# Kernel optimization log

Measured on AMD Instinct MI355X. Metric: run time of the kernel, lower is better.

## Reference

```python
import jax, jax.numpy as jnp
import numpy as np

B, T, D = 64, 256, 1024
H, HS = 16, 64
FF = 4096
EPS = 1e-5


def _layernorm(x, g, b):
    mu = jnp.mean(x, axis=-1, keepdims=True)
    var = jnp.mean(jnp.square(x - mu), axis=-1, keepdims=True)
    return (x - mu) * jax.lax.rsqrt(var + EPS) * g + b


def setup_inputs() -> dict:
    key = jax.random.key(0)
    ks = jax.random.split(key, 12)
    s = 0.02
    return {
        "x": jax.random.normal(ks[0], (B, T, D), jnp.float32),
        "ln1_g": jnp.ones((D,), jnp.float32),
        "ln1_b": jnp.zeros((D,), jnp.float32),
        "Wq": jax.random.normal(ks[1], (H, D, HS), jnp.float32) * s,
        "Wk": jax.random.normal(ks[2], (H, D, HS), jnp.float32) * s,
        "Wv": jax.random.normal(ks[3], (H, D, HS), jnp.float32) * s,
        "Wproj": jax.random.normal(ks[4], (D, D), jnp.float32) * s,
        "bproj": jnp.zeros((D,), jnp.float32),
        "ln2_g": jnp.ones((D,), jnp.float32),
        "ln2_b": jnp.zeros((D,), jnp.float32),
        "W1": jax.random.normal(ks[5], (D, FF), jnp.float32) * s,
        "b1": jnp.zeros((FF,), jnp.float32),
        "W2": jax.random.normal(ks[6], (FF, D), jnp.float32) * s,
        "b2": jnp.zeros((D,), jnp.float32),
    }


def reference(x, ln1_g, ln1_b, Wq, Wk, Wv, Wproj, bproj, ln2_g, ln2_b, W1, b1, W2, b2):
    # x = ln1(x)
    h = _layernorm(x, ln1_g, ln1_b)
    # per-head Q/K/V projections, batched over heads
    q = jnp.einsum("btd,hde->bhte", h, Wq)
    k = jnp.einsum("btd,hde->bhte", h, Wk)
    v = jnp.einsum("btd,hde->bhte", h, Wv)
    # NOTE: source scales by C**-0.5 with C = input_size (D), not head_size
    scale = D ** -0.5
    scores = jnp.einsum("bhte,bhse->bhts", q, k) * scale
    causal = jnp.tril(jnp.ones((T, T), bool))
    scores = jnp.where(causal, scores, -jnp.inf)
    w = jax.nn.softmax(scores, axis=-1)  # dropout is identity in eval
    attn = jnp.einsum("bhts,bhse->bthe", w, v).reshape(x.shape[0], x.shape[1], H * HS)
    sa = attn @ Wproj + bproj
    # residual onto ln1 output (as written in source)
    y = h + sa
    h2 = _layernorm(y, ln2_g, ln2_b)
    ff = jax.nn.relu(h2 @ W1 + b1) @ W2 + b2
    return h2 + ff
```

## Files before the change

kernel.cpp:

```cpp
#include <hip/hip_runtime.h>

typedef __bf16 bf16x8 __attribute__((ext_vector_type(8)));
typedef float f32x4 __attribute__((ext_vector_type(4)));
typedef unsigned short ushort_t;

__device__ __forceinline__ ushort_t f2bf(float f) {
  unsigned int u = __float_as_uint(f);
  u += 0x7fffu + ((u >> 16) & 1u);
  return (ushort_t)(u >> 16);
}

__device__ __forceinline__ void gl_lds16(const ushort_t* g, const char* l) {
  __builtin_amdgcn_global_load_lds(
      (const __attribute__((address_space(1))) void*)g,
      (__attribute__((address_space(3))) void*)l, 16, 0, 0);
}

__global__ __launch_bounds__(256) void fill_k(float* __restrict__ p, long n, float v) {
  long i = (long)blockIdx.x * 256 + threadIdx.x;
  if (i < n) p[i] = v;
}

__global__ __launch_bounds__(256) void transpose_w(const float* __restrict__ in,
                                                   ushort_t* __restrict__ out,
                                                   int R, int C) {
  __shared__ float tile[32][33];
  const float* inb = in + (long)blockIdx.z * R * C;
  ushort_t* outb = out + (long)blockIdx.z * R * C;
  int r0 = blockIdx.x * 32, c0 = blockIdx.y * 32;
  int tx = threadIdx.x & 31, ty = threadIdx.x >> 5;
#pragma unroll
  for (int i = ty; i < 32; i += 8) tile[i][tx] = inb[(long)(r0 + i) * C + (c0 + tx)];
  __syncthreads();
#pragma unroll
  for (int i = ty; i < 32; i += 8) outb[(long)(c0 + i) * R + (r0 + tx)] = f2bf(tile[tx][i]);
}

__global__ __launch_bounds__(256) void ln_k(const float* __restrict__ x,
                                            const float* __restrict__ g,
                                            const float* __restrict__ b,
                                            float* __restrict__ outF,
                                            ushort_t* __restrict__ outU) {
  __shared__ float red[8];
  long row = blockIdx.x;
  int tid = threadIdx.x;
  float4 v = ((const float4*)(x + row * 1024))[tid];
  float s = v.x + v.y + v.z + v.w;
#pragma unroll
  for (int off = 32; off; off >>= 1) s += __shfl_xor(s, off);
  int w = tid >> 6;
  if ((tid & 63) == 0) red[w] = s;
  __syncthreads();
  float mean = (red[0] + red[1] + red[2] + red[3]) * (1.0f / 1024.0f);
  float dx = v.x - mean, dy = v.y - mean, dz = v.z - mean, dw = v.w - mean;
  float s2 = dx * dx + dy * dy + dz * dz + dw * dw;
#pragma unroll
  for (int off = 32; off; off >>= 1) s2 += __shfl_xor(s2, off);
  if ((tid & 63) == 0) red[4 + w] = s2;
  __syncthreads();
  float var = (red[4] + red[5] + red[6] + red[7]) * (1.0f / 1024.0f);
  float rstd = rsqrtf(var + 1e-5f);
  int c = tid * 4;
  float o0 = dx * rstd * g[c + 0] + b[c + 0];
  float o1 = dy * rstd * g[c + 1] + b[c + 1];
  float o2 = dz * rstd * g[c + 2] + b[c + 2];
  float o3 = dw * rstd * g[c + 3] + b[c + 3];
  ((float4*)(outF + row * 1024))[tid] = make_float4(o0, o1, o2, o3);
  ushort4 u;
  u.x = f2bf(o0); u.y = f2bf(o1); u.z = f2bf(o2); u.w = f2bf(o3);
  ((ushort4*)(outU + row * 1024))[tid] = u;
}

template <int EPI>
__global__ __launch_bounds__(512, 2) void gemm256(const ushort_t* __restrict__ A,
                                                  const ushort_t* __restrict__ Bt,
                                                  int M, int N, int K, int NBC,
                                                  const float* __restrict__ bias,
                                                  const float* res, float* outF,
                                                  ushort_t* __restrict__ outU,
                                                  ushort_t* __restrict__ outU2,
                                                  ushort_t* __restrict__ outU3) {
  __shared__ __align__(16) char lds[131072];
  const int tid = threadIdx.x;
  const int lane = tid & 63;
  const int w = tid >> 6;
  const int wr = w >> 2, wc = w & 3;
  const int g = lane >> 4, lr = lane & 15;
  const int cpx = gridDim.x >> 3;
  const int wg = (blockIdx.x & 7) * cpx + (blockIdx.x >> 3);
  const long m0 = (long)(wg / NBC) * 256;
  const long n0 = (long)(wg % NBC) * 256;
  const int srow = tid >> 3;
  const int sslot = (tid & 7) ^ (srow & 7);
  const ushort_t* sA = A + (m0 + srow) * (long)K + sslot * 8;
  const ushort_t* sB = Bt + (n0 + srow) * (long)K + sslot * 8;
  const int dA = tid * 16;
  const int dB = 32768 + tid * 16;
  const int abase = (wr * 128 + lr) * 128;
  const int bbase = 32768 + (wc * 64 + lr) * 128;
  const int s0 = g ^ (lr & 7);
  const int s1 = (4 + g) ^ (lr & 7);
  const int NT = K >> 6;

  f32x4 acc[8][4] = {};
  bf16x8 aR[4][2], bR[4][2];
  const char* rb;

#define STAGE_A(tile, half) do {                                          \
    const long _ko = (long)(tile) * 64;                                   \
    char* _d = lds + (((tile) & 1) << 16) + ((half) << 14) + dA;          \
    gl_lds16(sA + _ko + (long)(2 * (half)) * 64 * K, _d);                 \
    gl_lds16(sA + _ko + (long)(2 * (half) + 1) * 64 * K, _d + 8192);      \
  } while (0)
#define STAGE_B(tile, half) do {                                          \
    const long _ko = (long)(tile) * 64;                                   \
    char* _d = lds + (((tile) & 1) << 16) + ((half) << 14) + dB;          \
    gl_lds16(sB + _ko + (long)(2 * (half)) * 64 * K, _d);                 \
    gl_lds16(sB + _ko + (long)(2 * (half) + 1) * 64 * K, _d + 8192);      \
  } while (0)
#define RD_A(base_mf) do {                                                \
    _Pragma("unroll") for (int mf = 0; mf < 4; ++mf) {                    \
      aR[mf][0] = *(const bf16x8*)(rb + abase + ((base_mf) + mf) * 2048 + s0 * 16); \
      aR[mf][1] = *(const bf16x8*)(rb + abase + ((base_mf) + mf) * 2048 + s1 * 16); \
    } } while (0)
#define RD_B2(base_nf) do {                                               \
    _Pragma("unroll") for (int nf = 0; nf < 2; ++nf) {                    \
      bR[(base_nf) + nf][0] = *(const bf16x8*)(rb + bbase + ((base_nf) + nf) * 2048 + s0 * 16); \
      bR[(base_nf) + nf][1] = *(const bf16x8*)(rb + bbase + ((base_nf) + nf) * 2048 + s1 * 16); \
    } } while (0)
#define QUAD(MB, NB) do {                                                 \
    __builtin_amdgcn_s_setprio(1);                                        \
    _Pragma("unroll") for (int mf = 0; mf < 4; ++mf)                      \
      _Pragma("unroll") for (int nf = 0; nf < 2; ++nf) {                  \
        acc[(MB) + mf][(NB) + nf] = __builtin_amdgcn_mfma_f32_16x16x32_bf16(aR[mf][0], bR[(NB) + nf][0], acc[(MB) + mf][(NB) + nf], 0, 0, 0); \
        acc[(MB) + mf][(NB) + nf] = __builtin_amdgcn_mfma_f32_16x16x32_bf16(aR[mf][1], bR[(NB) + nf][1], acc[(MB) + mf][(NB) + nf], 0, 0, 0); \
      }                                                                   \
    __builtin_amdgcn_s_setprio(0); } while (0)
#define LGKM0 do {                                                        \
    asm volatile("s_waitcnt lgkmcnt(0)" ::: "memory");                    \
    __builtin_amdgcn_sched_barrier(0); } while (0)

  STAGE_B(0, 0); STAGE_B(0, 1); STAGE_A(0, 0); STAGE_A(0, 1);
  STAGE_B(1, 0); STAGE_B(1, 1); STAGE_A(1, 0);
  asm volatile("s_waitcnt vmcnt(6)" ::: "memory");
  __builtin_amdgcn_s_barrier();

  for (int t = 0; t < NT; t += 2) {
    const bool s2 = (t + 2 < NT), s3 = (t + 3 < NT);
    rb = lds;
    RD_A(0);
    RD_B2(0);
    STAGE_A(t + 1, 1);
    asm volatile("s_waitcnt lgkmcnt(8)" ::: "memory");
    __builtin_amdgcn_s_barrier();
    LGKM0;
    QUAD(0, 0);
    __builtin_amdgcn_s_barrier();
    RD_B2(2);
    __builtin_amdgcn_s_barrier();
    LGKM0;
    QUAD(0, 2);
    __builtin_amdgcn_s_barrier();
    if (s2) STAGE_B(t + 2, 0);
    RD_A(4);
    __builtin_amdgcn_s_barrier();
    LGKM0;
    QUAD(4, 2);
    __builtin_amdgcn_s_barrier();
    if (s2) { STAGE_B(t + 2, 1); STAGE_A(t + 2, 0); }
    __builtin_amdgcn_s_barrier();
    QUAD(4, 0);
    if (s2) asm volatile("s_waitcnt vmcnt(6)" ::: "memory");
    else    asm volatile("s_waitcnt vmcnt(0)" ::: "memory");
    __builtin_amdgcn_s_barrier();
    rb = lds + 65536;
    RD_A(0);
    RD_B2(0);
    if (s2) STAGE_A(t + 2, 1);
    asm volatile("s_waitcnt lgkmcnt(8)" ::: "memory");
    __builtin_amdgcn_s_barrier();
    LGKM0;
    QUAD(0, 0);
    __builtin_amdgcn_s_barrier();
    RD_B2(2);
    __builtin_amdgcn_s_barrier();
    LGKM0;
    QUAD(0, 2);
    __builtin_amdgcn_s_barrier();
    if (s3) STAGE_B(t + 3, 0);
    RD_A(4);
    __builtin_amdgcn_s_barrier();
    LGKM0;
    QUAD(4, 2);
    __builtin_amdgcn_s_barrier();
    if (s3) { STAGE_B(t + 3, 1); STAGE_A(t + 3, 0); }
    __builtin_amdgcn_s_barrier();
    QUAD(4, 0);
    if (s3) asm volatile("s_waitcnt vmcnt(6)" ::: "memory");
    else    asm volatile("s_waitcnt vmcnt(0)" ::: "memory");
    __builtin_amdgcn_s_barrier();
  }
#undef STAGE_A
#undef STAGE_B
#undef RD_A
#undef RD_B2
#undef QUAD
#undef LGKM0

  if constexpr (EPI == 4) {
    const int p = (int)(n0 >> 10);
    const long bb2 = m0 >> 8;
    if (p < 2) {
      ushort_t* dst = (p == 0) ? outU : outU2;
#pragma unroll
      for (int mf = 0; mf < 8; ++mf)
#pragma unroll
        for (int nf = 0; nf < 4; ++nf)
#pragma unroll
          for (int r = 0; r < 4; ++r) {
            long tt = (wr * 128 + mf * 16 + g * 4 + r);
            long cc = (n0 & 1023) + wc * 64 + nf * 16 + lr;
            long hh = cc >> 6, e = cc & 63;
            dst[(((bb2 * 16 + hh) * 256 + tt) << 6) + e] = f2bf(acc[mf][nf][r]);
          }
    } else {
      unsigned int* l32 = (unsigned int*)lds;
#pragma unroll
      for (int mf = 0; mf < 8; ++mf)
#pragma unroll
        for (int nf = 0; nf < 4; ++nf)
#pragma unroll
          for (int r2 = 0; r2 < 2; ++r2) {
            int row = wr * 128 + mf * 16 + g * 4 + r2 * 2;
            int col = wc * 64 + nf * 16 + lr;
            unsigned int pk = (unsigned int)f2bf(acc[mf][nf][r2 * 2]) |
                              ((unsigned int)f2bf(acc[mf][nf][r2 * 2 + 1]) << 16);
            l32[col * 128 + ((row >> 1) ^ ((col & 7) << 2))] = pk;
          }
      __syncthreads();
      const long vcol0 = (n0 & 1023);
#pragma unroll
      for (int k = 0; k < 16; ++k) {
        int c = tid + k * 512;
        int e_l = c >> 5, k16 = c & 31;
        uint4 d = *(uint4*)&l32[e_l * 128 + ((k16 * 4) ^ ((e_l & 7) << 2))];
        long vc = vcol0 + e_l;
        long hh = vc >> 6, e = vc & 63;
        *(uint4*)&outU3[(((bb2 * 16 + hh) * 64 + e) << 8) + k16 * 8] = d;
      }
    }
  } else {
#pragma unroll
    for (int mf = 0; mf < 8; ++mf)
#pragma unroll
      for (int nf = 0; nf < 4; ++nf)
#pragma unroll
        for (int r = 0; r < 4; ++r) {
          long row = m0 + wr * 128 + mf * 16 + g * 4 + r;
          long col = n0 + wc * 64 + nf * 16 + lr;
          float v = acc[mf][nf][r];
          if constexpr (EPI == 2) {
            long i = row * N + col;
            outF[i] = v + bias[col] + res[i];
          } else {
            outU[row * N + col] = f2bf(fmaxf(v + bias[col], 0.0f));
          }
        }
  }
}

__global__ __launch_bounds__(64, 4) void attn_k(const ushort_t* __restrict__ q,
                                                const ushort_t* __restrict__ k,
                                                const ushort_t* __restrict__ vt,
                                                ushort_t* __restrict__ ao) {
  __shared__ __align__(16) ushort_t Ps[32][40];
  const int lane = threadIdx.x;
  const int g = lane >> 4, lr = lane & 15;
  const int blk = blockIdx.x;
  const int q8 = blk & 7;
  const int bh = blk >> 3;
  const int bb = bh >> 4, hh = bh & 15;
  const int q0 = q8 * 32;
  const ushort_t* qb = q + (long)bh * 256 * 64;
  const ushort_t* kb = k + (long)bh * 256 * 64;
  const ushort_t* vb = vt + (long)bh * 64 * 256;
  bf16x8 qf[2][2];
#pragma unroll
  for (int m = 0; m < 2; m++)
#pragma unroll
    for (int ks = 0; ks < 2; ks++)
      qf[m][ks] = *(const bf16x8*)(qb + (q0 + m * 16 + lr) * 64 + ks * 32 + g * 8);
  f32x4 o[2][4] = {};
  float mrow[2][4], lrow[2][4];
#pragma unroll
  for (int m = 0; m < 2; m++)
#pragma unroll
    for (int r = 0; r < 4; r++) { mrow[m][r] = -3.0e38f; lrow[m][r] = 0.0f; }
  const float sc2 = 0.04508422f;
  const int nkb = q8 + 1;
  for (int kbk = 0; kbk < nkb; kbk++) {
    f32x4 s[2][2] = {};
#pragma unroll
    for (int ks = 0; ks < 2; ks++) {
      bf16x8 kf[2];
#pragma unroll
      for (int n = 0; n < 2; n++)
        kf[n] = *(const bf16x8*)(kb + (kbk * 32 + n * 16 + lr) * 64 + ks * 32 + g * 8);
#pragma unroll
      for (int m = 0; m < 2; m++)
#pragma unroll
        for (int n = 0; n < 2; n++)
          s[m][n] = __builtin_amdgcn_mfma_f32_16x16x32_bf16(qf[m][ks], kf[n], s[m][n], 0, 0, 0);
    }
    bf16x8 vf[4];
#pragma unroll
    for (int n = 0; n < 4; n++)
      vf[n] = *(const bf16x8*)(vb + (n * 16 + lr) * 256 + kbk * 32 + g * 8);
    if (kbk == q8) {
#pragma unroll
      for (int m = 0; m < 2; m++)
#pragma unroll
        for (int n = 0; n < 2; n++)
#pragma unroll
          for (int r = 0; r < 4; r++) {
            int row = q0 + m * 16 + g * 4 + r;
            int col = kbk * 32 + n * 16 + lr;
            s[m][n][r] = (col <= row) ? s[m][n][r] * sc2 : -3.0e38f;
          }
    } else {
#pragma unroll
      for (int m = 0; m < 2; m++)
#pragma unroll
        for (int n = 0; n < 2; n++)
#pragma unroll
          for (int r = 0; r < 4; r++) s[m][n][r] *= sc2;
    }
    float mx[2][4];
    float growth = -3.0e38f;
#pragma unroll
    for (int m = 0; m < 2; m++)
#pragma unroll
      for (int r = 0; r < 4; r++) {
        float v = fmaxf(s[m][0][r], s[m][1][r]);
#pragma unroll
        for (int off = 8; off; off >>= 1) v = fmaxf(v, __shfl_xor(v, off));
        mx[m][r] = v;
        growth = fmaxf(growth, v - mrow[m][r]);
      }
    if (__any(growth > 8.0f)) {
#pragma unroll
      for (int m = 0; m < 2; m++)
#pragma unroll
        for (int r = 0; r < 4; r++) {
          float mn = fmaxf(mrow[m][r], mx[m][r]);
          float al = exp2f(mrow[m][r] - mn);
          mrow[m][r] = mn;
          lrow[m][r] *= al;
#pragma unroll
          for (int n = 0; n < 4; n++) o[m][n][r] *= al;
        }
    }
#pragma unroll
    for (int m = 0; m < 2; m++)
#pragma unroll
      for (int r = 0; r < 4; r++) {
        float rs = 0.0f;
#pragma unroll
        for (int n = 0; n < 2; n++) {
          float p = exp2f(s[m][n][r] - mrow[m][r]);
          s[m][n][r] = p;
          rs += p;
        }
#pragma unroll
        for (int off = 8; off; off >>= 1) rs += __shfl_xor(rs, off);
        lrow[m][r] += rs;
      }
#pragma unroll
    for (int m = 0; m < 2; m++)
#pragma unroll
      for (int n = 0; n < 2; n++)
#pragma unroll
        for (int r = 0; r < 4; r++)
          Ps[m * 16 + g * 4 + r][n * 16 + lr] = f2bf(s[m][n][r]);
#pragma unroll
    for (int m = 0; m < 2; m++) {
      bf16x8 pa = *(const bf16x8*)&Ps[m * 16 + lr][g * 8];
#pragma unroll
      for (int n = 0; n < 4; n++)
        o[m][n] = __builtin_amdgcn_mfma_f32_16x16x32_bf16(pa, vf[n], o[m][n], 0, 0, 0);
    }
  }
#pragma unroll
  for (int m = 0; m < 2; m++)
#pragma unroll
    for (int r = 0; r < 4; r++) {
      float inv = 1.0f / lrow[m][r];
      long t = q0 + m * 16 + g * 4 + r;
#pragma unroll
      for (int n = 0; n < 4; n++) {
        long e = n * 16 + lr;
        ao[((long)bb * 256 + t) * 1024 + hh * 64 + e] = f2bf(o[m][n][r] * inv);
      }
    }
}

extern "C" void kernel_launch(void* const* d_in, const int* in_sizes, int n_in,
                              void* d_out, int out_size, void* d_ws, size_t ws_size,
                              hipStream_t stream) {
  const float* x     = (const float*)d_in[0];
  const float* ln1g  = (const float*)d_in[1];
  const float* ln1b  = (const float*)d_in[2];
  const float* Wq    = (const float*)d_in[3];
  const float* Wk    = (const float*)d_in[4];
  const float* Wv    = (const float*)d_in[5];
  const float* Wproj = (const float*)d_in[6];
  const float* bproj = (const float*)d_in[7];
  const float* ln2g  = (const float*)d_in[8];
  const float* ln2b  = (const float*)d_in[9];
  const float* W1    = (const float*)d_in[10];
  const float* b1    = (const float*)d_in[11];
  const float* W2    = (const float*)d_in[12];
  const float* b2    = (const float*)d_in[13];

  const long NEED = 184L << 20;
  if (ws_size < (size_t)NEED) {
    fill_k<<<(out_size + 255) / 256, 256, 0, stream>>>((float*)d_out, out_size,
                                                       (float)(ws_size >> 20));
    return;
  }

  char* ws = (char*)d_ws;
  const long MB = 1 << 20;
  ushort_t* wqt = (ushort_t*)(ws + 0 * MB);
  ushort_t* wkt = (ushort_t*)(ws + 2 * MB);
  ushort_t* wvt = (ushort_t*)(ws + 4 * MB);
  ushort_t* wpt = (ushort_t*)(ws + 6 * MB);
  ushort_t* w1t = (ushort_t*)(ws + 8 * MB);
  ushort_t* w2t = (ushort_t*)(ws + 16 * MB);
  ushort_t* hb  = (ushort_t*)(ws + 24 * MB);
  ushort_t* qbf = (ushort_t*)(ws + 56 * MB);
  ushort_t* kbf = (ushort_t*)(ws + 88 * MB);
  ushort_t* vtb = (ushort_t*)(ws + 120 * MB);
  ushort_t* atb = (ushort_t*)(ws + 152 * MB);
  ushort_t* ff1 = (ushort_t*)(ws + 56 * MB);
  float*    yf  = (float*)d_out;

  transpose_w<<<dim3(32, 2, 16), 256, 0, stream>>>(Wq, wqt, 1024, 64);
  transpose_w<<<dim3(32, 2, 16), 256, 0, stream>>>(Wk, wkt, 1024, 64);
  transpose_w<<<dim3(32, 2, 16), 256, 0, stream>>>(Wv, wvt, 1024, 64);
  transpose_w<<<dim3(32, 32, 1), 256, 0, stream>>>(Wproj, wpt, 1024, 1024);
  transpose_w<<<dim3(32, 128, 1), 256, 0, stream>>>(W1, w1t, 1024, 4096);
  transpose_w<<<dim3(128, 32, 1), 256, 0, stream>>>(W2, w2t, 4096, 1024);

  ln_k<<<16384, 256, 0, stream>>>(x, ln1g, ln1b, yf, hb);
  gemm256<4><<<768, 512, 0, stream>>>(hb, wqt, 16384, 3072, 1024, 12,
                                      nullptr, nullptr, nullptr, qbf, kbf, vtb);
  attn_k<<<8192, 64, 0, stream>>>(qbf, kbf, vtb, atb);
  gemm256<2><<<256, 512, 0, stream>>>(atb, wpt, 16384, 1024, 1024, 4,
                                      bproj, yf, yf, nullptr, nullptr, nullptr);
  ln_k<<<16384, 256, 0, stream>>>(yf, ln2g, ln2b, yf, hb);
  gemm256<3><<<1024, 512, 0, stream>>>(hb, w1t, 16384, 4096, 1024, 16,
                                       b1, nullptr, nullptr, ff1, nullptr, nullptr);
  gemm256<2><<<256, 512, 0, stream>>>(ff1, w2t, 16384, 1024, 4096, 4,
                                      b2, yf, yf, nullptr, nullptr, nullptr);
}
```

Before: 638.0 us.

## Keep residual stream in bf16 and stage GEMM epilogues through LDS

The fp32 residual copies written by layernorm and the projection GEMM are replaced with bf16 tensors: LN1 writes only bf16, the proj GEMM adds the bf16 residual and emits bf16, LN2 reads bf16, and the final GEMM adds the bf16 LN2 output as residual. The ReLU and proj epilogues, and the Q/K output epilogue, now stage tiles in swizzled LDS and write 16-byte coalesced stores instead of scattered 2-byte stores. This cuts HBM traffic and uncoalesced writes at the cost of extra rounding of the residual paths to bf16.

```diff
diff --git a/kernel.cpp b/kernel.cpp
--- a/kernel.cpp
+++ b/kernel.cpp
@@ -8,6 +8,9 @@
   unsigned int u = __float_as_uint(f);
   u += 0x7fffu + ((u >> 16) & 1u);
   return (ushort_t)(u >> 16);
+}
+__device__ __forceinline__ float bf2f(ushort_t u) {
+  return __uint_as_float(((unsigned int)u) << 16);
 }
 
 __device__ __forceinline__ void gl_lds16(const ushort_t* g, const char* l) {
@@ -36,15 +39,21 @@
   for (int i = ty; i < 32; i += 8) outb[(long)(c0 + i) * R + (r0 + tx)] = f2bf(tile[tx][i]);
 }
 
-__global__ __launch_bounds__(256) void ln_k(const float* __restrict__ x,
+template <bool BFIN>
+__global__ __launch_bounds__(256) void ln_k(const void* __restrict__ xin,
                                             const float* __restrict__ g,
                                             const float* __restrict__ b,
-                                            float* __restrict__ outF,
                                             ushort_t* __restrict__ outU) {
   __shared__ float red[8];
   long row = blockIdx.x;
   int tid = threadIdx.x;
-  float4 v = ((const float4*)(x + row * 1024))[tid];
+  float4 v;
+  if constexpr (BFIN) {
+    ushort4 u4 = ((const ushort4*)((const ushort_t*)xin + row * 1024))[tid];
+    v = make_float4(bf2f(u4.x), bf2f(u4.y), bf2f(u4.z), bf2f(u4.w));
+  } else {
+    v = ((const float4*)((const float*)xin + row * 1024))[tid];
+  }
   float s = v.x + v.y + v.z + v.w;
 #pragma unroll
   for (int off = 32; off; off >>= 1) s += __shfl_xor(s, off);
@@ -61,13 +70,11 @@
   float var = (red[4] + red[5] + red[6] + red[7]) * (1.0f / 1024.0f);
   float rstd = rsqrtf(var + 1e-5f);
   int c = tid * 4;
-  float o0 = dx * rstd * g[c + 0] + b[c + 0];
-  float o1 = dy * rstd * g[c + 1] + b[c + 1];
-  float o2 = dz * rstd * g[c + 2] + b[c + 2];
-  float o3 = dw * rstd * g[c + 3] + b[c + 3];
-  ((float4*)(outF + row * 1024))[tid] = make_float4(o0, o1, o2, o3);
   ushort4 u;
-  u.x = f2bf(o0); u.y = f2bf(o1); u.z = f2bf(o2); u.w = f2bf(o3);
+  u.x = f2bf(dx * rstd * g[c + 0] + b[c + 0]);
+  u.y = f2bf(dy * rstd * g[c + 1] + b[c + 1]);
+  u.z = f2bf(dz * rstd * g[c + 2] + b[c + 2]);
+  u.w = f2bf(dw * rstd * g[c + 3] + b[c + 3]);
   ((ushort4*)(outU + row * 1024))[tid] = u;
 }
 
@@ -76,7 +83,8 @@
                                                   const ushort_t* __restrict__ Bt,
                                                   int M, int N, int K, int NBC,
                                                   const float* __restrict__ bias,
-                                                  const float* res, float* outF,
+                                                  const ushort_t* __restrict__ resU,
+                                                  float* __restrict__ outF,
                                                   ushort_t* __restrict__ outU,
                                                   ushort_t* __restrict__ outU2,
                                                   ushort_t* __restrict__ outU3) {
@@ -207,22 +215,72 @@
 #undef QUAD
 #undef LGKM0
 
-  if constexpr (EPI == 4) {
+  if constexpr (EPI == 3 || EPI == 5) {
+    ushort_t* l16 = (ushort_t*)lds;
+#pragma unroll
+    for (int mf = 0; mf < 8; ++mf)
+#pragma unroll
+      for (int nf = 0; nf < 4; ++nf) {
+        int col = wc * 64 + nf * 16 + lr;
+        long gcol = n0 + col;
+#pragma unroll
+        for (int r = 0; r < 4; ++r) {
+          int row = wr * 128 + mf * 16 + g * 4 + r;
+          float v = acc[mf][nf][r] + bias[gcol];
+          if constexpr (EPI == 3) v = fmaxf(v, 0.0f);
+          else v += bf2f(resU[(m0 + row) * (long)N + gcol]);
+          l16[row * 256 + (col ^ (g << 3))] = f2bf(v);
+        }
+      }
+    __syncthreads();
+#pragma unroll
+    for (int k = 0; k < 16; ++k) {
+      int c = tid + k * 512;
+      int tt = c >> 5, off = c & 31;
+      int pc = (off * 8) ^ ((((unsigned)tt >> 2) & 3) << 3);
+      uint4 d = *(uint4*)&l16[tt * 256 + pc];
+      *(uint4*)&outU[(m0 + tt) * (long)N + n0 + off * 8] = d;
+    }
+  } else if constexpr (EPI == 6) {
+#pragma unroll
+    for (int mf = 0; mf < 8; ++mf)
+#pragma unroll
+      for (int nf = 0; nf < 4; ++nf)
+#pragma unroll
+        for (int r = 0; r < 4; ++r) {
+          long row = m0 + wr * 128 + mf * 16 + g * 4 + r;
+          long col = n0 + wc * 64 + nf * 16 + lr;
+          long i = row * (long)N + col;
+          outF[i] = acc[mf][nf][r] + bias[col] + bf2f(resU[i]);
+        }
+  } else {
     const int p = (int)(n0 >> 10);
     const long bb2 = m0 >> 8;
     if (p < 2) {
       ushort_t* dst = (p == 0) ? outU : outU2;
+      ushort_t* l16 = (ushort_t*)lds;
 #pragma unroll
       for (int mf = 0; mf < 8; ++mf)
 #pragma unroll
-        for (int nf = 0; nf < 4; ++nf)
+        for (int nf = 0; nf < 4; ++nf) {
+          int col = wc * 64 + nf * 16 + lr;
 #pragma unroll
           for (int r = 0; r < 4; ++r) {
-            long tt = (wr * 128 + mf * 16 + g * 4 + r);
-            long cc = (n0 & 1023) + wc * 64 + nf * 16 + lr;
-            long hh = cc >> 6, e = cc & 63;
-            dst[(((bb2 * 16 + hh) * 256 + tt) << 6) + e] = f2bf(acc[mf][nf][r]);
+            int row = wr * 128 + mf * 16 + g * 4 + r;
+            l16[row * 256 + (col ^ (g << 3))] = f2bf(acc[mf][nf][r]);
           }
+        }
+      __syncthreads();
+      const int hh0 = (int)((n0 & 1023) >> 6);
+#pragma unroll
+      for (int k = 0; k < 16; ++k) {
+        int c = tid + k * 512;
+        int hh_l = c >> 11, tt = (c >> 3) & 255, off = c & 7;
+        int col = hh_l * 64 + off * 8;
+        int pc = col ^ ((((unsigned)tt >> 2) & 3) << 3);
+        uint4 d = *(uint4*)&l16[tt * 256 + pc];
+        *(uint4*)&dst[(((bb2 * 16 + hh0 + hh_l) * 256 + tt) << 6) + off * 8] = d;
+      }
     } else {
       unsigned int* l32 = (unsigned int*)lds;
 #pragma unroll
@@ -249,23 +307,6 @@
         *(uint4*)&outU3[(((bb2 * 16 + hh) * 64 + e) << 8) + k16 * 8] = d;
       }
     }
-  } else {
-#pragma unroll
-    for (int mf = 0; mf < 8; ++mf)
-#pragma unroll
-      for (int nf = 0; nf < 4; ++nf)
-#pragma unroll
-        for (int r = 0; r < 4; ++r) {
-          long row = m0 + wr * 128 + mf * 16 + g * 4 + r;
-          long col = n0 + wc * 64 + nf * 16 + lr;
-          float v = acc[mf][nf][r];
-          if constexpr (EPI == 2) {
-            long i = row * N + col;
-            outF[i] = v + bias[col] + res[i];
-          } else {
-            outU[row * N + col] = f2bf(fmaxf(v + bias[col], 0.0f));
-          }
-        }
   }
 }
 
@@ -442,8 +483,8 @@
   ushort_t* kbf = (ushort_t*)(ws + 88 * MB);
   ushort_t* vtb = (ushort_t*)(ws + 120 * MB);
   ushort_t* atb = (ushort_t*)(ws + 152 * MB);
+  ushort_t* yb  = (ushort_t*)(ws + 56 * MB);
   ushort_t* ff1 = (ushort_t*)(ws + 56 * MB);
-  float*    yf  = (float*)d_out;
 
   transpose_w<<<dim3(32, 2, 16), 256, 0, stream>>>(Wq, wqt, 1024, 64);
   transpose_w<<<dim3(32, 2, 16), 256, 0, stream>>>(Wk, wkt, 1024, 64);
@@ -452,15 +493,15 @@
   transpose_w<<<dim3(32, 128, 1), 256, 0, stream>>>(W1, w1t, 1024, 4096);
   transpose_w<<<dim3(128, 32, 1), 256, 0, stream>>>(W2, w2t, 4096, 1024);
 
-  ln_k<<<16384, 256, 0, stream>>>(x, ln1g, ln1b, yf, hb);
+  ln_k<false><<<16384, 256, 0, stream>>>(x, ln1g, ln1b, hb);
   gemm256<4><<<768, 512, 0, stream>>>(hb, wqt, 16384, 3072, 1024, 12,
                                       nullptr, nullptr, nullptr, qbf, kbf, vtb);
   attn_k<<<8192, 64, 0, stream>>>(qbf, kbf, vtb, atb);
-  gemm256<2><<<256, 512, 0, stream>>>(atb, wpt, 16384, 1024, 1024, 4,
-                                      bproj, yf, yf, nullptr, nullptr, nullptr);
-  ln_k<<<16384, 256, 0, stream>>>(yf, ln2g, ln2b, yf, hb);
+  gemm256<5><<<256, 512, 0, stream>>>(atb, wpt, 16384, 1024, 1024, 4,
+                                      bproj, hb, nullptr, yb, nullptr, nullptr);
+  ln_k<true><<<16384, 256, 0, stream>>>(yb, ln2g, ln2b, hb);
   gemm256<3><<<1024, 512, 0, stream>>>(hb, w1t, 16384, 4096, 1024, 16,
                                        b1, nullptr, nullptr, ff1, nullptr, nullptr);
-  gemm256<2><<<256, 512, 0, stream>>>(ff1, w2t, 16384, 1024, 4096, 4,
-                                      b2, yf, yf, nullptr, nullptr, nullptr);
-}
+  gemm256<6><<<256, 512, 0, stream>>>(ff1, w2t, 16384, 1024, 4096, 4,
+                                      b2, hb, (float*)d_out, nullptr, nullptr, nullptr);
+}
```

Result: faster. 595.8 us (-6.6%).
